# Performance work log

Hardware: AMD Instinct MI355X
Metric: run time of the kernel (lower is better)

## Reference

```python
import jax, jax.numpy as jnp
import numpy as np

HEADS = 16
MAX_DIST = 1024

def setup_inputs() -> dict:
    key = jax.random.key(0)
    k1, k2, k3, k4 = jax.random.split(key, 4)
    b, n, dim = 2, 2048, 1024
    x = jax.random.normal(k1, (b, n, dim), dtype=jnp.float32)
    W_qkv = jax.random.normal(k2, (3 * dim, dim), dtype=jnp.float32) * (dim ** -0.5)
    W_out = jax.random.normal(k3, (dim, dim), dtype=jnp.float32) * (dim ** -0.5)
    b_out = jnp.zeros((dim,), dtype=jnp.float32)
    rel_emb = jax.random.normal(k4, (2 * MAX_DIST + 1, HEADS), dtype=jnp.float32) * 0.02
    return {"x": x, "W_qkv": W_qkv, "W_out": W_out, "b_out": b_out, "rel_emb": rel_emb}

def reference(x, W_qkv, W_out, b_out, rel_emb):
    b, n, dim = x.shape
    h = HEADS
    d = dim // h
    scale = d ** -0.5
    qkv = jnp.einsum('bnd,ed->bne', x, W_qkv)  # [b, n, 3*dim]
    q, k, v = jnp.split(qkv, 3, axis=-1)
    def to_heads(t):
        return t.reshape(b, n, h, d).transpose(0, 2, 1, 3)  # b h n d
    q, k, v = to_heads(q), to_heads(k), to_heads(v)
    # relative position bias: [1, h, n, n]
    dist = jnp.arange(n)[None, :] - jnp.arange(n)[:, None]
    idx = jnp.clip(dist, -MAX_DIST, MAX_DIST) + MAX_DIST  # [n, n]
    rel_bias = rel_emb[idx].transpose(2, 0, 1)[None]  # [1, h, n, n]
    scores = jnp.einsum('bhqd,bhkd->bhqk', q, k) * scale + rel_bias
    attn = jax.nn.softmax(scores, axis=-1)
    out = jnp.einsum('bhqk,bhkd->bhqd', attn, v)
    out = out.transpose(0, 2, 1, 3).reshape(b, n, dim)
    return jnp.einsum('bnd,ed->bne', out, W_out) + b_out
```

## Files before the change

### kernel.cpp

```cpp
#include <hip/hip_runtime.h>
#include <hip/hip_bf16.h>

typedef __attribute__((ext_vector_type(8))) short short8;
typedef __attribute__((ext_vector_type(4))) float f32x4;
typedef __attribute__((ext_vector_type(16))) float f32x16;
typedef __attribute__((ext_vector_type(4))) unsigned short u16x4;
typedef __attribute__((ext_vector_type(2))) unsigned int u32x2;
typedef __attribute__((ext_vector_type(4))) unsigned int u32x4;
typedef __hip_bfloat16 bf16;

#define SCALE_Q 0.18033688f

#define GLD_LDS16(g, l) __builtin_amdgcn_global_load_lds(                      \
    (const __attribute__((address_space(1))) void*)(g),                        \
    (__attribute__((address_space(3))) void*)(l), 16, 0, 0)

static __device__ __forceinline__ f32x4 mfma16(short8 a, short8 b, f32x4 c) {
  return __builtin_amdgcn_mfma_f32_16x16x32_bf16(a, b, c, 0, 0, 0);
}
static __device__ __forceinline__ f32x16 mfma32(short8 a, short8 b, f32x16 c) {
  return __builtin_amdgcn_mfma_f32_32x32x16_bf16(a, b, c, 0, 0, 0);
}

static __device__ __forceinline__ unsigned cvtpk(float lo, float hi) {
  unsigned r;
  asm("v_cvt_pk_bf16_f32 %0, %1, %2" : "=v"(r) : "v"(lo), "v"(hi));
  return r;
}

static __device__ __forceinline__ float fexp2(float x) {
  float r;
  asm("v_exp_f32 %0, %1" : "=v"(r) : "v"(x));
  return r;
}

#define PLSWAP(a, b) asm("v_permlane32_swap_b32 %0, %1" : "+v"(a), "+v"(b))

__global__ __launch_bounds__(256) void k_pre(
    const float* __restrict__ x, const float* __restrict__ Wqkv,
    const float* __restrict__ Wout, const float* __restrict__ rel,
    bf16* __restrict__ xb, bf16* __restrict__ wqb, bf16* __restrict__ wob,
    float* __restrict__ relpf) {
  int bid = blockIdx.x;
  if (bid < 8192) {
    const float* in;
    bf16* out;
    long i;
    if (bid < 4096) {
      in = x; out = xb; i = (long)bid * 256 + threadIdx.x;
    } else if (bid < 7168) {
      in = Wqkv; out = wqb; i = (long)(bid - 4096) * 256 + threadIdx.x;
    } else {
      in = Wout; out = wob; i = (long)(bid - 7168) * 256 + threadIdx.x;
    }
    f32x4 v = *(const f32x4*)(in + i * 4);
    u16x4 o;
#pragma unroll
    for (int j = 0; j < 4; ++j)
      o[j] = __builtin_bit_cast(unsigned short, __float2bfloat16(v[j]));
    *(u16x4*)((unsigned short*)out + i * 4) = o;
  } else {
    int base = (bid - 8192) * 1024 + threadIdx.x;
#pragma unroll
    for (int k = 0; k < 4; ++k) {
      int i = base + k * 256;
      int h = i >> 12, ii = i & 4095;
      int dd = ii - 2047;
      dd = dd < -1024 ? -1024 : (dd > 1024 ? 1024 : dd);
      relpf[i] = rel[(size_t)(dd + 1024) * 16 + h] * 1.44269504f - 16.0f;
    }
  }
}

__global__ __launch_bounds__(256, 3) void k_gemm(
    const bf16* __restrict__ A, const bf16* __restrict__ B,
    int M, int N, int K, int epi,
    bf16* __restrict__ Qb, bf16* __restrict__ Kb, bf16* __restrict__ Vb,
    float* __restrict__ Out, const float* __restrict__ bias) {
  __shared__ bf16 lA[3][4096];
  __shared__ bf16 lB[3][4096];
  const int tid = threadIdx.x, w = tid >> 6, l = tid & 63;
  const int m0 = blockIdx.x * 128, n0 = blockIdx.y * 128;
  const int wrow = (w >> 1) * 64, wcol = (w & 1) * 64;
  const int fr = l & 15, fq = l >> 4;
  f32x4 acc[4][4] = {};
  const int c0 = w * 64 + l, c1 = c0 + 256;
  const bf16* Ag0 = A + (size_t)(m0 + (c0 >> 2)) * K + (c0 & 3) * 8;
  const bf16* Ag1 = A + (size_t)(m0 + (c1 >> 2)) * K + (c1 & 3) * 8;
  const bf16* Bg0 = B + (size_t)(n0 + (c0 >> 2)) * K + (c0 & 3) * 8;
  const bf16* Bg1 = B + (size_t)(n0 + (c1 >> 2)) * K + (c1 & 3) * 8;
  bf16* lA0 = &lA[0][w * 512];
  bf16* lA1 = &lA[0][2048 + w * 512];
  bf16* lB0 = &lB[0][w * 512];
  bf16* lB1 = &lB[0][2048 + w * 512];

#define GSTAGE(T, BI)                                                          \
  do {                                                                         \
    const int ko_ = (T) * 32;                                                  \
    GLD_LDS16(Ag0 + ko_, lA0 + (BI) * 4096);                                   \
    GLD_LDS16(Ag1 + ko_, lA1 + (BI) * 4096);                                   \
    GLD_LDS16(Bg0 + ko_, lB0 + (BI) * 4096);                                   \
    GLD_LDS16(Bg1 + ko_, lB1 + (BI) * 4096);                                   \
  } while (0)

  const int nk = K >> 5;
  GSTAGE(0, 0);
  __builtin_amdgcn_sched_barrier(0);
  GSTAGE(1, 1);
  __builtin_amdgcn_sched_barrier(0);

  int bc_ = 0, bs_ = 2;
  for (int t = 0; t < nk; ++t) {
    asm volatile("s_waitcnt vmcnt(4)" ::: "memory");
    __builtin_amdgcn_s_barrier();
    __builtin_amdgcn_sched_barrier(0);
    int tt = (t + 2 < nk) ? t + 2 : nk - 1;
    GSTAGE(tt, bs_);
    __builtin_amdgcn_sched_barrier(0);
    const bf16* pA = &lA[bc_][0];
    const bf16* pB = &lB[bc_][0];
    short8 af[4], bfv[4];
#pragma unroll
    for (int mi = 0; mi < 4; ++mi)
      af[mi] = *(const short8*)&pA[(wrow + mi * 16 + fr) * 32 + fq * 8];
#pragma unroll
    for (int ni = 0; ni < 4; ++ni)
      bfv[ni] = *(const short8*)&pB[(wcol + ni * 16 + fr) * 32 + fq * 8];
    __builtin_amdgcn_s_setprio(1);
#pragma unroll
    for (int mi = 0; mi < 4; ++mi)
#pragma unroll
      for (int ni = 0; ni < 4; ++ni)
        acc[mi][ni] = mfma16(bfv[ni], af[mi], acc[mi][ni]);
    __builtin_amdgcn_s_setprio(0);
    bc_ = (bc_ == 2) ? 0 : bc_ + 1;
    bs_ = (bs_ == 2) ? 0 : bs_ + 1;
  }
#undef GSTAGE

  if (epi == 0) {
#pragma unroll
    for (int mi = 0; mi < 4; ++mi)
#pragma unroll
      for (int ni = 0; ni < 4; ++ni) {
        int t = m0 + wrow + mi * 16 + fr;
        int e4 = n0 + wcol + ni * 16 + fq * 4;
        int sect = e4 >> 10, eh = (e4 >> 6) & 15, dh = e4 & 63;
        int b = t >> 11, tt = t & 2047;
        size_t idx = (((size_t)b * 16 + eh) * 2048 + tt) * 64 + dh;
        f32x4 a = acc[mi][ni];
        float sc = (sect == 0) ? SCALE_Q : 1.f;
        u32x2 ov;
        ov[0] = cvtpk(a[0] * sc, a[1] * sc);
        ov[1] = cvtpk(a[2] * sc, a[3] * sc);
        bf16* dst = (sect == 0) ? Qb : (sect == 1) ? Kb : Vb;
        *(u32x2*)(dst + idx) = ov;
      }
  } else {
#pragma unroll
    for (int mi = 0; mi < 4; ++mi)
#pragma unroll
      for (int ni = 0; ni < 4; ++ni) {
        int t = m0 + wrow + mi * 16 + fr;
        int e4 = n0 + wcol + ni * 16 + fq * 4;
        f32x4 bv = *(const f32x4*)(bias + e4);
        f32x4 a = acc[mi][ni];
        f32x4 o = {a[0] + bv[0], a[1] + bv[1], a[2] + bv[2], a[3] + bv[3]};
        *(f32x4*)(Out + (size_t)t * N + e4) = o;
      }
  }
}

__global__ __launch_bounds__(256) void k_trv(const bf16* __restrict__ Vb,
                                             bf16* __restrict__ Vt) {
  __shared__ bf16 tile[64][80];
  const int bh = blockIdx.y, t0 = blockIdx.x * 64;
  const int tid = threadIdx.x;
#pragma unroll
  for (int it = 0; it < 2; ++it) {
    int idx = tid + it * 256;
    int r = idx >> 3, c8 = (idx & 7) * 8;
    short8 v = *(const short8*)(Vb + ((size_t)bh * 2048 + t0 + r) * 64 + c8);
    *(short8*)&tile[r][c8] = v;
  }
  __syncthreads();
#pragma unroll
  for (int it = 0; it < 2; ++it) {
    int idx = tid + it * 256;
    int d = idx >> 3, c8 = (idx & 7) * 8;
    short8 o;
#pragma unroll
    for (int j = 0; j < 8; ++j)
      o[j] = __builtin_bit_cast(short, tile[c8 + j][d]);
    *(short8*)(Vt + ((size_t)bh * 64 + d) * 2048 + t0 + c8) = o;
  }
}

__global__ __launch_bounds__(256, 2) void k_attn(
    const bf16* __restrict__ Qb, const bf16* __restrict__ Kb,
    const bf16* __restrict__ Vt, const float* __restrict__ relpf,
    bf16* __restrict__ AO) {
  __shared__ bf16 lK[2][8192];
  __shared__ bf16 lV[2][8192];

  const int id = blockIdx.x;
  const int xcd = id & 7, j = id >> 3;
  const int bh = xcd * 4 + (j >> 4), qt = j & 15;
  const int h = bh & 15, b = bh >> 4;
  const int tid = threadIdx.x, w = tid >> 6, l = tid & 63;
  const int r32 = l & 31, hl = l >> 5, rs7 = r32 & 7;
  const int q0w = qt * 128 + w * 32;

  const bf16* Kbh = Kb + (size_t)bh * 2048 * 64;
  const bf16* Vbh = Vt + (size_t)bh * 64 * 2048;
  const bf16* Ks[4];
  const bf16* Vs[4];
#pragma unroll
  for (int s = 0; s < 4; ++s) {
    int c = tid + 256 * s;
    int kr = c >> 3, kc = (c & 7) ^ (kr & 7);
    Ks[s] = Kbh + (size_t)kr * 64 + kc * 8;
    int vr = c >> 4, vc = (c & 15) ^ (vr & 7);
    Vs[s] = Vbh + (size_t)vr * 2048 + vc * 8;
  }

#define STAGE(KT, BI)                                                          \
  do {                                                                         \
    _Pragma("unroll") for (int s = 0; s < 4; ++s) {                            \
      GLD_LDS16(Ks[s] + (size_t)(KT) * 64, &lK[BI][(tid + 256 * s) * 8]);      \
      GLD_LDS16(Vs[s] + (KT), &lV[BI][(tid + 256 * s) * 8]);                   \
    }                                                                          \
  } while (0)

  const bf16* Qp = Qb + ((size_t)bh * 2048 + q0w + r32) * 64;
  short8 qf[4];
#pragma unroll
  for (int ks = 0; ks < 4; ++ks)
    qf[ks] = *(const short8*)(Qp + ks * 16 + hl * 8);

  const float* bp = relpf + h * 4096 + (2047 + 4 * hl - q0w - r32);

  float llane = 0.f;
  f32x16 o0 = {}, o1 = {};

  STAGE(0, 0);
  __builtin_amdgcn_sched_barrier(0);

  int cur = 0;
  for (int t = 0; t < 16; ++t) {
    const int kt = t * 128;
    asm volatile("s_waitcnt vmcnt(0)" ::: "memory");
    __builtin_amdgcn_s_barrier();
    __builtin_amdgcn_sched_barrier(0);
    f32x16 bc[4];
#pragma unroll
    for (int kb = 0; kb < 4; ++kb)
#pragma unroll
      for (int reg = 0; reg < 16; ++reg)
        bc[kb][reg] = bp[kt + kb * 32 + (reg & 3) + 8 * (reg >> 2)];
    __builtin_amdgcn_sched_barrier(0);
    if (t < 15) STAGE(kt + 128, cur ^ 1);
    __builtin_amdgcn_sched_barrier(0);
    const bf16* lKc = &lK[cur][0];
    const bf16* lVc = &lV[cur][0];
    f32x16 s[4] = {};
    __builtin_amdgcn_s_setprio(1);
#pragma unroll
    for (int kb = 0; kb < 4; ++kb)
#pragma unroll
      for (int ks = 0; ks < 4; ++ks) {
        short8 kf = *(const short8*)&lKc[(kb * 32 + r32) * 64 +
                                         (((2 * ks + hl) ^ rs7) * 8)];
        s[kb] = mfma32(kf, qf[ks], s[kb]);
      }
    __builtin_amdgcn_s_setprio(0);
    float ra[4] = {0.f, 0.f, 0.f, 0.f};
#pragma unroll
    for (int kb = 0; kb < 4; ++kb)
#pragma unroll
      for (int reg = 0; reg < 16; ++reg) {
        float e = fexp2(s[kb][reg] + bc[kb][reg]);
        s[kb][reg] = e;
        ra[reg & 3] += e;
      }
    llane += (ra[0] + ra[1]) + (ra[2] + ra[3]);
#pragma unroll
    for (int kb = 0; kb < 4; ++kb) {
#pragma unroll
      for (int kh = 0; kh < 2; ++kh) {
        const int e = kh * 8;
        unsigned a0 = cvtpk(s[kb][e + 0], s[kb][e + 1]);
        unsigned a1 = cvtpk(s[kb][e + 2], s[kb][e + 3]);
        unsigned b0 = cvtpk(s[kb][e + 4], s[kb][e + 5]);
        unsigned b1 = cvtpk(s[kb][e + 6], s[kb][e + 7]);
        PLSWAP(a0, b0);
        PLSWAP(a1, b1);
        u32x4 pw = {a0, a1, b0, b1};
        short8 pf = __builtin_bit_cast(short8, pw);
        const int ks = kb * 2 + kh;
        const int cc = ((2 * ks + hl) ^ rs7) * 8;
        short8 v0 = *(const short8*)&lVc[r32 * 128 + cc];
        short8 v1 = *(const short8*)&lVc[(32 + r32) * 128 + cc];
        __builtin_amdgcn_s_setprio(1);
        o0 = mfma32(v0, pf, o0);
        o1 = mfma32(v1, pf, o1);
        __builtin_amdgcn_s_setprio(0);
      }
    }
    cur ^= 1;
  }
#undef STAGE

  float lsum = llane + __shfl_xor(llane, 32);
  float rin = 1.f / lsum;
  bf16* aor = AO + ((size_t)(b * 2048 + q0w + r32)) * 1024 + h * 64 + hl * 4;
#pragma unroll
  for (int rg = 0; rg < 4; ++rg) {
    u32x2 ov0, ov1;
    ov0[0] = cvtpk(o0[4 * rg + 0] * rin, o0[4 * rg + 1] * rin);
    ov0[1] = cvtpk(o0[4 * rg + 2] * rin, o0[4 * rg + 3] * rin);
    *(u32x2*)(aor + rg * 8) = ov0;
    ov1[0] = cvtpk(o1[4 * rg + 0] * rin, o1[4 * rg + 1] * rin);
    ov1[1] = cvtpk(o1[4 * rg + 2] * rin, o1[4 * rg + 3] * rin);
    *(u32x2*)(aor + 32 + rg * 8) = ov1;
  }
}

extern "C" void kernel_launch(void* const* d_in, const int* in_sizes, int n_in,
                              void* d_out, int out_size, void* d_ws,
                              size_t ws_size, hipStream_t stream) {
  const float* x = (const float*)d_in[0];
  const float* Wqkv = (const float*)d_in[1];
  const float* Wout = (const float*)d_in[2];
  const float* bout = (const float*)d_in[3];
  const float* rel = (const float*)d_in[4];
  float* out = (float*)d_out;

  char* p = (char*)d_ws;
  bf16* xb  = (bf16*)(p);
  bf16* wqb = (bf16*)(p + (8ull << 20));
  bf16* wob = (bf16*)(p + (14ull << 20));
  bf16* Qb  = (bf16*)(p + (16ull << 20));
  bf16* Kb  = (bf16*)(p + (24ull << 20));
  bf16* Vb  = (bf16*)(p + (32ull << 20));
  bf16* Vt  = (bf16*)(p + (40ull << 20));
  bf16* aob = (bf16*)(p + (48ull << 20));
  float* relpf = (float*)(p + (56ull << 20));

  k_pre<<<8256, 256, 0, stream>>>(x, Wqkv, Wout, rel, xb, wqb, wob, relpf);
  k_gemm<<<dim3(32, 24), 256, 0, stream>>>(xb, wqb, 4096, 3072, 1024, 0,
                                           Qb, Kb, Vb, nullptr, nullptr);
  k_trv<<<dim3(32, 32), 256, 0, stream>>>(Vb, Vt);
  k_attn<<<512, 256, 0, stream>>>(Qb, Kb, Vt, relpf, aob);
  k_gemm<<<dim3(32, 8), 256, 0, stream>>>(aob, wob, 4096, 1024, 1024, 1,
                                          nullptr, nullptr, nullptr, out, bout);
}
```

Before: 128.5 us.

## Fuse V transpose into QKV GEMM epilogue and software-pipeline attention QK with PV

The QKV GEMM epilogue now writes V directly in transposed layout with scattered 2-byte stores, which removes the separate transpose kernel and its extra global round trip. The attention kernel is restructured to compute the next tile's QK^T scores while the current tile does softmax and PV. It prefetches two tiles ahead using a triple-buffered V in LDS and vectorized bias loads. The costs are uncoalesced scalar stores in the GEMM, more registers for two score sets, and more LDS, all of which could hurt occupancy.

```diff
diff --git a/kernel.cpp b/kernel.cpp
--- a/kernel.cpp
+++ b/kernel.cpp
@@ -4,6 +4,7 @@
 typedef __attribute__((ext_vector_type(8))) short short8;
 typedef __attribute__((ext_vector_type(4))) float f32x4;
 typedef __attribute__((ext_vector_type(16))) float f32x16;
+typedef float f32x4u __attribute__((ext_vector_type(4), aligned(4)));
 typedef __attribute__((ext_vector_type(4))) unsigned short u16x4;
 typedef __attribute__((ext_vector_type(2))) unsigned int u32x2;
 typedef __attribute__((ext_vector_type(4))) unsigned int u32x4;
@@ -75,7 +76,7 @@
 __global__ __launch_bounds__(256, 3) void k_gemm(
     const bf16* __restrict__ A, const bf16* __restrict__ B,
     int M, int N, int K, int epi,
-    bf16* __restrict__ Qb, bf16* __restrict__ Kb, bf16* __restrict__ Vb,
+    bf16* __restrict__ Qb, bf16* __restrict__ Kb, bf16* __restrict__ Vt,
     float* __restrict__ Out, const float* __restrict__ bias) {
   __shared__ bf16 lA[3][4096];
   __shared__ bf16 lB[3][4096];
@@ -147,14 +148,25 @@
         int e4 = n0 + wcol + ni * 16 + fq * 4;
         int sect = e4 >> 10, eh = (e4 >> 6) & 15, dh = e4 & 63;
         int b = t >> 11, tt = t & 2047;
-        size_t idx = (((size_t)b * 16 + eh) * 2048 + tt) * 64 + dh;
         f32x4 a = acc[mi][ni];
-        float sc = (sect == 0) ? SCALE_Q : 1.f;
-        u32x2 ov;
-        ov[0] = cvtpk(a[0] * sc, a[1] * sc);
-        ov[1] = cvtpk(a[2] * sc, a[3] * sc);
-        bf16* dst = (sect == 0) ? Qb : (sect == 1) ? Kb : Vb;
-        *(u32x2*)(dst + idx) = ov;
+        if (sect < 2) {
+          size_t idx = (((size_t)b * 16 + eh) * 2048 + tt) * 64 + dh;
+          float sc = (sect == 0) ? SCALE_Q : 1.f;
+          u32x2 ov;
+          ov[0] = cvtpk(a[0] * sc, a[1] * sc);
+          ov[1] = cvtpk(a[2] * sc, a[3] * sc);
+          bf16* dst = (sect == 0) ? Qb : Kb;
+          *(u32x2*)(dst + idx) = ov;
+        } else {
+          size_t vb = ((size_t)((b << 4) + eh) * 64 + dh) * 2048 + tt;
+          unsigned p0 = cvtpk(a[0], a[1]);
+          unsigned p1 = cvtpk(a[2], a[3]);
+          unsigned short* vp = (unsigned short*)Vt;
+          vp[vb] = (unsigned short)p0;
+          vp[vb + 2048] = (unsigned short)(p0 >> 16);
+          vp[vb + 4096] = (unsigned short)p1;
+          vp[vb + 6144] = (unsigned short)(p1 >> 16);
+        }
       }
   } else {
 #pragma unroll
@@ -171,37 +183,12 @@
   }
 }
 
-__global__ __launch_bounds__(256) void k_trv(const bf16* __restrict__ Vb,
-                                             bf16* __restrict__ Vt) {
-  __shared__ bf16 tile[64][80];
-  const int bh = blockIdx.y, t0 = blockIdx.x * 64;
-  const int tid = threadIdx.x;
-#pragma unroll
-  for (int it = 0; it < 2; ++it) {
-    int idx = tid + it * 256;
-    int r = idx >> 3, c8 = (idx & 7) * 8;
-    short8 v = *(const short8*)(Vb + ((size_t)bh * 2048 + t0 + r) * 64 + c8);
-    *(short8*)&tile[r][c8] = v;
-  }
-  __syncthreads();
-#pragma unroll
-  for (int it = 0; it < 2; ++it) {
-    int idx = tid + it * 256;
-    int d = idx >> 3, c8 = (idx & 7) * 8;
-    short8 o;
-#pragma unroll
-    for (int j = 0; j < 8; ++j)
-      o[j] = __builtin_bit_cast(short, tile[c8 + j][d]);
-    *(short8*)(Vt + ((size_t)bh * 64 + d) * 2048 + t0 + c8) = o;
-  }
-}
-
 __global__ __launch_bounds__(256, 2) void k_attn(
     const bf16* __restrict__ Qb, const bf16* __restrict__ Kb,
     const bf16* __restrict__ Vt, const float* __restrict__ relpf,
     bf16* __restrict__ AO) {
   __shared__ bf16 lK[2][8192];
-  __shared__ bf16 lV[2][8192];
+  __shared__ bf16 lV[3][8192];
 
   const int id = blockIdx.x;
   const int xcd = id & 7, j = id >> 3;
@@ -224,92 +211,123 @@
     Vs[s] = Vbh + (size_t)vr * 2048 + vc * 8;
   }
 
-#define STAGE(KT, BI)                                                          \
+#define STAGEK(KT, BP)                                                         \
   do {                                                                         \
-    _Pragma("unroll") for (int s = 0; s < 4; ++s) {                            \
-      GLD_LDS16(Ks[s] + (size_t)(KT) * 64, &lK[BI][(tid + 256 * s) * 8]);      \
-      GLD_LDS16(Vs[s] + (KT), &lV[BI][(tid + 256 * s) * 8]);                   \
+    _Pragma("unroll") for (int s_ = 0; s_ < 4; ++s_)                           \
+        GLD_LDS16(Ks[s_] + (size_t)(KT) * 64, (BP) + (tid + 256 * s_) * 8);    \
+  } while (0)
+#define STAGEV(KT, BP)                                                         \
+  do {                                                                         \
+    _Pragma("unroll") for (int s_ = 0; s_ < 4; ++s_)                           \
+        GLD_LDS16(Vs[s_] + (KT), (BP) + (tid + 256 * s_) * 8);                 \
+  } while (0)
+
+  const bf16* Qp = Qb + ((size_t)bh * 2048 + q0w + r32) * 64;
+  short8 qf[4];
+#pragma unroll
+  for (int ks = 0; ks < 4; ++ks)
+    qf[ks] = *(const short8*)(Qp + ks * 16 + hl * 8);
+
+  const float* bp = relpf + h * 4096 + (2047 + 4 * hl - q0w - r32);
+
+  float llane = 0.f;
+  f32x16 o0 = {}, o1 = {};
+  f32x16 sA[4], sB[4];
+
+  STAGEK(0, &lK[0][0]);
+  STAGEV(0, &lV[0][0]);
+  __builtin_amdgcn_sched_barrier(0);
+  STAGEK(128, &lK[1][0]);
+  STAGEV(128, &lV[1][0]);
+  __builtin_amdgcn_sched_barrier(0);
+  asm volatile("s_waitcnt vmcnt(8)" ::: "memory");
+  __builtin_amdgcn_s_barrier();
+  __builtin_amdgcn_sched_barrier(0);
+#pragma unroll
+  for (int kb = 0; kb < 4; ++kb) sA[kb] = (f32x16){};
+  __builtin_amdgcn_s_setprio(1);
+#pragma unroll
+  for (int kb = 0; kb < 4; ++kb)
+#pragma unroll
+    for (int ks = 0; ks < 4; ++ks) {
+      short8 kf = *(const short8*)&lK[0][(kb * 32 + r32) * 64 +
+                                         (((2 * ks + hl) ^ rs7) * 8)];
+      sA[kb] = mfma32(kf, qf[ks], sA[kb]);
+    }
+  __builtin_amdgcn_s_setprio(0);
+
+#define ITER(T, SC, SN)                                                        \
+  do {                                                                         \
+    const int t_ = (T);                                                        \
+    const int kt_ = t_ * 128;                                                  \
+    asm volatile("s_waitcnt vmcnt(0)" ::: "memory");      \
+    __builtin_amdgcn_s_barrier();                                              \
+    __builtin_amdgcn_sched_barrier(0);                                         \
+    f32x4u bcv[4][4];                                                          \
+    _Pragma("unroll") for (int kb = 0; kb < 4; ++kb)                           \
+        _Pragma("unroll") for (int g = 0; g < 4; ++g)                          \
+            bcv[kb][g] = *(const f32x4u*)(bp + kt_ + kb * 32 + 8 * g);         \
+    __builtin_amdgcn_sched_barrier(0);                                         \
+    {                                                                          \
+      int ts_ = t_ + 2 > 15 ? 15 : t_ + 2;   \
+      STAGEK(ts_ * 128, &lK[t_ & 1][0]);                                       \
+      STAGEV(ts_ * 128, &lV[(t_ + 2) % 3][0]);                                 \
+    }                                                                          \
+    __builtin_amdgcn_sched_barrier(0);                                         \
+    if (t_ < 15) {                    \
+      const bf16* lKn = &lK[(t_ + 1) & 1][0];                                  \
+      _Pragma("unroll") for (int kb = 0; kb < 4; ++kb) SN[kb] = (f32x16){};    \
+      __builtin_amdgcn_s_setprio(1);                                           \
+      _Pragma("unroll") for (int kb = 0; kb < 4; ++kb)                         \
+          _Pragma("unroll") for (int ks = 0; ks < 4; ++ks) {                   \
+        short8 kf = *(const short8*)&lKn[(kb * 32 + r32) * 64 +                \
+                                         (((2 * ks + hl) ^ rs7) * 8)];         \
+        SN[kb] = mfma32(kf, qf[ks], SN[kb]);                                   \
+      }                                                                        \
+      __builtin_amdgcn_s_setprio(0);                                           \
+    }                                                                          \
+    const bf16* lVc = &lV[t_ % 3][0];                                          \
+    float ra0 = 0.f, ra1 = 0.f, ra2 = 0.f, ra3 = 0.f;                          \
+    _Pragma("unroll") for (int kb = 0; kb < 4; ++kb)                           \
+        _Pragma("unroll") for (int reg = 0; reg < 16; ++reg) {                 \
+      float e_ = fexp2(SC[kb][reg] + bcv[kb][reg >> 2][reg & 3]);              \
+      SC[kb][reg] = e_;                                                        \
+      if ((reg & 3) == 0) ra0 += e_;                                           \
+      else if ((reg & 3) == 1) ra1 += e_;                                      \
+      else if ((reg & 3) == 2) ra2 += e_;                                      \
+      else ra3 += e_;                                                          \
+    }                                                                          \
+    llane += (ra0 + ra1) + (ra2 + ra3);                                        \
+    _Pragma("unroll") for (int kb = 0; kb < 4; ++kb) {                         \
+      _Pragma("unroll") for (int kh = 0; kh < 2; ++kh) {                       \
+        const int e = kh * 8;                                                  \
+        unsigned a0 = cvtpk(SC[kb][e + 0], SC[kb][e + 1]);                     \
+        unsigned a1 = cvtpk(SC[kb][e + 2], SC[kb][e + 3]);                     \
+        unsigned b0 = cvtpk(SC[kb][e + 4], SC[kb][e + 5]);                     \
+        unsigned b1 = cvtpk(SC[kb][e + 6], SC[kb][e + 7]);                     \
+        PLSWAP(a0, b0);             \
+        PLSWAP(a1, b1);                                                        \
+        u32x4 pw = {a0, a1, b0, b1};                                           \
+        short8 pf = __builtin_bit_cast(short8, pw);                            \
+        const int ks = kb * 2 + kh;                                            \
+        const int cc = ((2 * ks + hl) ^ rs7) * 8;                              \
+        short8 v0 = *(const short8*)&lVc[r32 * 128 + cc];                      \
+        short8 v1 = *(const short8*)&lVc[(32 + r32) * 128 + cc];               \
+        __builtin_amdgcn_s_setprio(1);                                         \
+        o0 = mfma32(v0, pf, o0);                                               \
+        o1 = mfma32(v1, pf, o1);                                               \
+        __builtin_amdgcn_s_setprio(0);                                         \
+      }                                                                        \
     }                                                                          \
   } while (0)
 
-  const bf16* Qp = Qb + ((size_t)bh * 2048 + q0w + r32) * 64;
-  short8 qf[4];
-#pragma unroll
-  for (int ks = 0; ks < 4; ++ks)
-    qf[ks] = *(const short8*)(Qp + ks * 16 + hl * 8);
-
-  const float* bp = relpf + h * 4096 + (2047 + 4 * hl - q0w - r32);
-
-  float llane = 0.f;
-  f32x16 o0 = {}, o1 = {};
-
-  STAGE(0, 0);
-  __builtin_amdgcn_sched_barrier(0);
-
-  int cur = 0;
-  for (int t = 0; t < 16; ++t) {
-    const int kt = t * 128;
-    asm volatile("s_waitcnt vmcnt(0)" ::: "memory");
-    __builtin_amdgcn_s_barrier();
-    __builtin_amdgcn_sched_barrier(0);
-    f32x16 bc[4];
-#pragma unroll
-    for (int kb = 0; kb < 4; ++kb)
-#pragma unroll
-      for (int reg = 0; reg < 16; ++reg)
-        bc[kb][reg] = bp[kt + kb * 32 + (reg & 3) + 8 * (reg >> 2)];
-    __builtin_amdgcn_sched_barrier(0);
-    if (t < 15) STAGE(kt + 128, cur ^ 1);
-    __builtin_amdgcn_sched_barrier(0);
-    const bf16* lKc = &lK[cur][0];
-    const bf16* lVc = &lV[cur][0];
-    f32x16 s[4] = {};
-    __builtin_amdgcn_s_setprio(1);
-#pragma unroll
-    for (int kb = 0; kb < 4; ++kb)
-#pragma unroll
-      for (int ks = 0; ks < 4; ++ks) {
-        short8 kf = *(const short8*)&lKc[(kb * 32 + r32) * 64 +
-                                         (((2 * ks + hl) ^ rs7) * 8)];
-        s[kb] = mfma32(kf, qf[ks], s[kb]);
-      }
-    __builtin_amdgcn_s_setprio(0);
-    float ra[4] = {0.f, 0.f, 0.f, 0.f};
-#pragma unroll
-    for (int kb = 0; kb < 4; ++kb)
-#pragma unroll
-      for (int reg = 0; reg < 16; ++reg) {
-        float e = fexp2(s[kb][reg] + bc[kb][reg]);
-        s[kb][reg] = e;
-        ra[reg & 3] += e;
-      }
-    llane += (ra[0] + ra[1]) + (ra[2] + ra[3]);
-#pragma unroll
-    for (int kb = 0; kb < 4; ++kb) {
-#pragma unroll
-      for (int kh = 0; kh < 2; ++kh) {
-        const int e = kh * 8;
-        unsigned a0 = cvtpk(s[kb][e + 0], s[kb][e + 1]);
-        unsigned a1 = cvtpk(s[kb][e + 2], s[kb][e + 3]);
-        unsigned b0 = cvtpk(s[kb][e + 4], s[kb][e + 5]);
-        unsigned b1 = cvtpk(s[kb][e + 6], s[kb][e + 7]);
-        PLSWAP(a0, b0);
-        PLSWAP(a1, b1);
-        u32x4 pw = {a0, a1, b0, b1};
-        short8 pf = __builtin_bit_cast(short8, pw);
-        const int ks = kb * 2 + kh;
-        const int cc = ((2 * ks + hl) ^ rs7) * 8;
-        short8 v0 = *(const short8*)&lVc[r32 * 128 + cc];
-        short8 v1 = *(const short8*)&lVc[(32 + r32) * 128 + cc];
-        __builtin_amdgcn_s_setprio(1);
-        o0 = mfma32(v0, pf, o0);
-        o1 = mfma32(v1, pf, o1);
-        __builtin_amdgcn_s_setprio(0);
-      }
-    }
-    cur ^= 1;
-  }
-#undef STAGE
+  for (int tt = 0; tt < 8; ++tt) {
+    ITER(2 * tt, sA, sB);
+    ITER(2 * tt + 1, sB, sA);
+  }
+#undef ITER
+#undef STAGEK
+#undef STAGEV
 
   float lsum = llane + __shfl_xor(llane, 32);
   float rin = 1.f / lsum;
@@ -342,16 +360,14 @@
   bf16* wob = (bf16*)(p + (14ull << 20));
   bf16* Qb  = (bf16*)(p + (16ull << 20));
   bf16* Kb  = (bf16*)(p + (24ull << 20));
-  bf16* Vb  = (bf16*)(p + (32ull << 20));
-  bf16* Vt  = (bf16*)(p + (40ull << 20));
-  bf16* aob = (bf16*)(p + (48ull << 20));
-  float* relpf = (float*)(p + (56ull << 20));
+  bf16* Vtr = (bf16*)(p + (32ull << 20));
+  bf16* aob = (bf16*)(p + (40ull << 20));
+  float* relpf = (float*)(p + (48ull << 20));
 
   k_pre<<<8256, 256, 0, stream>>>(x, Wqkv, Wout, rel, xb, wqb, wob, relpf);
   k_gemm<<<dim3(32, 24), 256, 0, stream>>>(xb, wqb, 4096, 3072, 1024, 0,
-                                           Qb, Kb, Vb, nullptr, nullptr);
-  k_trv<<<dim3(32, 32), 256, 0, stream>>>(Vb, Vt);
-  k_attn<<<512, 256, 0, stream>>>(Qb, Kb, Vt, relpf, aob);
+                                           Qb, Kb, Vtr, nullptr, nullptr);
+  k_attn<<<512, 256, 0, stream>>>(Qb, Kb, Vtr, relpf, aob);
   k_gemm<<<dim3(32, 8), 256, 0, stream>>>(aob, wob, 4096, 1024, 1024, 1,
                                           nullptr, nullptr, nullptr, out, bout);
 }
```

Result: slower. 249.1 us (+93.8%).

## Fuse V transpose into QKV GEMM epilogue and vectorize bias loads

Applied to the files above, without the earlier changes.

The QKV GEMM epilogue now writes V directly in the transposed [bh][d][t] layout that the attention kernel consumes, so the separate transpose kernel and its intermediate buffer are gone. The relative-bias loads in the attention loop are also grouped into 4-wide vector loads instead of scalar loads. This saves one kernel launch and a full read and write of V, but V is now stored as scattered 2-byte writes at a 4 KB stride, which coalesce poorly.

```diff
diff --git a/kernel.cpp b/kernel.cpp
--- a/kernel.cpp
+++ b/kernel.cpp
@@ -4,6 +4,7 @@
 typedef __attribute__((ext_vector_type(8))) short short8;
 typedef __attribute__((ext_vector_type(4))) float f32x4;
 typedef __attribute__((ext_vector_type(16))) float f32x16;
+typedef float f32x4u __attribute__((ext_vector_type(4), aligned(4)));
 typedef __attribute__((ext_vector_type(4))) unsigned short u16x4;
 typedef __attribute__((ext_vector_type(2))) unsigned int u32x2;
 typedef __attribute__((ext_vector_type(4))) unsigned int u32x4;
@@ -75,7 +76,7 @@
 __global__ __launch_bounds__(256, 3) void k_gemm(
     const bf16* __restrict__ A, const bf16* __restrict__ B,
     int M, int N, int K, int epi,
-    bf16* __restrict__ Qb, bf16* __restrict__ Kb, bf16* __restrict__ Vb,
+    bf16* __restrict__ Qb, bf16* __restrict__ Kb, bf16* __restrict__ Vt,
     float* __restrict__ Out, const float* __restrict__ bias) {
   __shared__ bf16 lA[3][4096];
   __shared__ bf16 lB[3][4096];
@@ -147,14 +148,25 @@
         int e4 = n0 + wcol + ni * 16 + fq * 4;
         int sect = e4 >> 10, eh = (e4 >> 6) & 15, dh = e4 & 63;
         int b = t >> 11, tt = t & 2047;
-        size_t idx = (((size_t)b * 16 + eh) * 2048 + tt) * 64 + dh;
         f32x4 a = acc[mi][ni];
-        float sc = (sect == 0) ? SCALE_Q : 1.f;
-        u32x2 ov;
-        ov[0] = cvtpk(a[0] * sc, a[1] * sc);
-        ov[1] = cvtpk(a[2] * sc, a[3] * sc);
-        bf16* dst = (sect == 0) ? Qb : (sect == 1) ? Kb : Vb;
-        *(u32x2*)(dst + idx) = ov;
+        if (sect < 2) {
+          size_t idx = (((size_t)b * 16 + eh) * 2048 + tt) * 64 + dh;
+          float sc = (sect == 0) ? SCALE_Q : 1.f;
+          u32x2 ov;
+          ov[0] = cvtpk(a[0] * sc, a[1] * sc);
+          ov[1] = cvtpk(a[2] * sc, a[3] * sc);
+          bf16* dst = (sect == 0) ? Qb : Kb;
+          *(u32x2*)(dst + idx) = ov;
+        } else {
+          size_t vb = ((size_t)((b << 4) + eh) * 64 + dh) * 2048 + tt;
+          unsigned p0 = cvtpk(a[0], a[1]);
+          unsigned p1 = cvtpk(a[2], a[3]);
+          unsigned short* vp = (unsigned short*)Vt;
+          vp[vb] = (unsigned short)p0;
+          vp[vb + 2048] = (unsigned short)(p0 >> 16);
+          vp[vb + 4096] = (unsigned short)p1;
+          vp[vb + 6144] = (unsigned short)(p1 >> 16);
+        }
       }
   } else {
 #pragma unroll
@@ -171,31 +183,6 @@
   }
 }
 
-__global__ __launch_bounds__(256) void k_trv(const bf16* __restrict__ Vb,
-                                             bf16* __restrict__ Vt) {
-  __shared__ bf16 tile[64][80];
-  const int bh = blockIdx.y, t0 = blockIdx.x * 64;
-  const int tid = threadIdx.x;
-#pragma unroll
-  for (int it = 0; it < 2; ++it) {
-    int idx = tid + it * 256;
-    int r = idx >> 3, c8 = (idx & 7) * 8;
-    short8 v = *(const short8*)(Vb + ((size_t)bh * 2048 + t0 + r) * 64 + c8);
-    *(short8*)&tile[r][c8] = v;
-  }
-  __syncthreads();
-#pragma unroll
-  for (int it = 0; it < 2; ++it) {
-    int idx = tid + it * 256;
-    int d = idx >> 3, c8 = (idx & 7) * 8;
-    short8 o;
-#pragma unroll
-    for (int j = 0; j < 8; ++j)
-      o[j] = __builtin_bit_cast(short, tile[c8 + j][d]);
-    *(short8*)(Vt + ((size_t)bh * 64 + d) * 2048 + t0 + c8) = o;
-  }
-}
-
 __global__ __launch_bounds__(256, 2) void k_attn(
     const bf16* __restrict__ Qb, const bf16* __restrict__ Kb,
     const bf16* __restrict__ Vt, const float* __restrict__ relpf,
@@ -256,8 +243,11 @@
 #pragma unroll
     for (int kb = 0; kb < 4; ++kb)
 #pragma unroll
-      for (int reg = 0; reg < 16; ++reg)
-        bc[kb][reg] = bp[kt + kb * 32 + (reg & 3) + 8 * (reg >> 2)];
+      for (int g = 0; g < 4; ++g) {
+        f32x4u v = *(const f32x4u*)(bp + kt + kb * 32 + 8 * g);
+#pragma unroll
+        for (int e = 0; e < 4; ++e) bc[kb][g * 4 + e] = v[e];
+      }
     __builtin_amdgcn_sched_barrier(0);
     if (t < 15) STAGE(kt + 128, cur ^ 1);
     __builtin_amdgcn_sched_barrier(0);
@@ -342,16 +332,14 @@
   bf16* wob = (bf16*)(p + (14ull << 20));
   bf16* Qb  = (bf16*)(p + (16ull << 20));
   bf16* Kb  = (bf16*)(p + (24ull << 20));
-  bf16* Vb  = (bf16*)(p + (32ull << 20));
-  bf16* Vt  = (bf16*)(p + (40ull << 20));
-  bf16* aob = (bf16*)(p + (48ull << 20));
-  float* relpf = (float*)(p + (56ull << 20));
+  bf16* Vtr = (bf16*)(p + (32ull << 20));
+  bf16* aob = (bf16*)(p + (40ull << 20));
+  float* relpf = (float*)(p + (48ull << 20));
 
   k_pre<<<8256, 256, 0, stream>>>(x, Wqkv, Wout, rel, xb, wqb, wob, relpf);
   k_gemm<<<dim3(32, 24), 256, 0, stream>>>(xb, wqb, 4096, 3072, 1024, 0,
-                                           Qb, Kb, Vb, nullptr, nullptr);
-  k_trv<<<dim3(32, 32), 256, 0, stream>>>(Vb, Vt);
-  k_attn<<<512, 256, 0, stream>>>(Qb, Kb, Vt, relpf, aob);
+                                           Qb, Kb, Vtr, nullptr, nullptr);
+  k_attn<<<512, 256, 0, stream>>>(Qb, Kb, Vtr, relpf, aob);
   k_gemm<<<dim3(32, 8), 256, 0, stream>>>(aob, wob, 4096, 1024, 1024, 1,
                                           nullptr, nullptr, nullptr, out, bout);
 }
```

Measured after the change: 122.3 us. -4.8%, faster.
